# Kernel optimization log

Hardware: AMD Instinct MI355X
Metric: run time of the kernel (lower is better)

Reference implementation:

```python
import jax, jax.numpy as jnp
import numpy as np

DEFAULT_MASK_VALUE = -0.7 * float(jnp.finfo(jnp.dtype('float32')).max)


def setup_inputs() -> dict:
    key = jax.random.key(0)
    k1, k2, k3, k4 = jax.random.split(key, 4)
    B, T, NQ, NKV, D = 2, 2048, 32, 8, 128
    query = jax.random.normal(k1, (B, T, NQ, D), dtype=jnp.float32)
    k = jax.random.normal(k2, (B, T, NKV, D), dtype=jnp.float32)
    v = jax.random.normal(k3, (B, T, NKV, D), dtype=jnp.float32)
    # packed-sequence segment ids: sorted small ints so segments are contiguous
    decoder_segment_ids = jnp.sort(jax.random.randint(k4, (B, T), 0, 4), axis=-1).astype(jnp.int32)
    return {"query": query, "key": k, "value": v, "decoder_segment_ids": decoder_segment_ids}


def _generate_attention_mask(q_seq_len, kv_seq_len, decoder_segment_ids):
    # segment mask: [b, 1, 1, t, s]
    seg = (decoder_segment_ids[:, :, None] == decoder_segment_ids[:, None, :])[:, None, None, :, :]
    # causal mask: [1, 1, 1, t, s]
    row = jax.lax.broadcasted_iota(jnp.int32, (q_seq_len, kv_seq_len), 0)
    col = jax.lax.broadcasted_iota(jnp.int32, (q_seq_len, kv_seq_len), 1)
    causal = (col <= row)[None, None, None, :, :]
    mask = jnp.logical_and(seg, causal)
    return jnp.where(mask, 0.0, DEFAULT_MASK_VALUE)


def _apply_mask_to_logits(logits, mask):
    return jnp.where(mask >= DEFAULT_MASK_VALUE * 0.5, logits, DEFAULT_MASK_VALUE)


def reference(query, key, value, decoder_segment_ids):
    b, t, n, d = query.shape
    n_kv = key.shape[2]
    g = n // n_kv  # query heads per kv head (GQA)
    q = query.reshape(b, t, n_kv, g, d)
    # qk product (no internal sqrt(d) scaling, matching AttentionOp.qk_product)
    logits = jnp.einsum('btkgd,bskd->bkgts', q, key)  # [b, n_kv, g, t, s]
    mask = _generate_attention_mask(t, key.shape[1], decoder_segment_ids)
    logits = _apply_mask_to_logits(logits, mask)
    weights = jax.nn.softmax(logits, axis=-1).astype(query.dtype)
    out = jnp.einsum('bkgts,bskd->btkgd', weights, value)
    return out.reshape(b, t, n, d)
```

## Files before the change

### kernel.cpp

```cpp
#include <hip/hip_runtime.h>


typedef __bf16 bf16x8 __attribute__((ext_vector_type(8)));
typedef _Float16 f16x8 __attribute__((ext_vector_type(8)));
typedef float f32x4 __attribute__((ext_vector_type(4)));

#define B_   2
#define T_   2048
#define NQ_  32
#define NKV_ 8
#define D_   128

#define MASKV (-3.0e38f)
#define LOG2E 1.44269504f
#define TILE_US 8192
#define WS_TILES_BYTES ((size_t)B_ * NKV_ * (T_ / 32) * TILE_US * 2)
#define WS_NEED (WS_TILES_BYTES + (size_t)B_ * T_ * 4)

static __device__ __forceinline__ unsigned short f2bf(float x) {
    union { float f; unsigned int u; } c; c.f = x;
    unsigned int r = c.u + 0x7fffu + ((c.u >> 16) & 1u);
    return (unsigned short)(r >> 16);
}

union U8  { unsigned short us[8]; bf16x8 v; };
union H8  { _Float16 h[8]; f16x8 v; };

static __device__ __forceinline__ void dma16(const unsigned short* g, unsigned short* l) {
    __builtin_amdgcn_global_load_lds(
        (const __attribute__((address_space(1))) unsigned int*)g,
        (__attribute__((address_space(3))) unsigned int*)l, 16, 0, 0);
}

__global__ __launch_bounds__(256)
void prep(const float* __restrict__ kg, const float* __restrict__ vg,
          unsigned short* __restrict__ ws)
{
    const int tid = threadIdx.x;
    const int st  = blockIdx.x;
    const int kvh = blockIdx.y;
    const int b   = blockIdx.z;
    unsigned short* base = ws + ((size_t)((b * NKV_ + kvh) * (T_ / 32) + st)) * TILE_US;

    #pragma unroll
    for (int it = 0; it < 2; ++it) {
        int task = tid + it * 256;
        int r = task >> 4, c = task & 15;
        const float* kp = kg + (((size_t)(b * T_ + st * 32 + r)) * NKV_ + kvh) * D_ + c * 8;
        H8 hu;
        #pragma unroll
        for (int j = 0; j < 8; ++j) hu.h[j] = (_Float16)kp[j];
        int slot = r * 16 + (c ^ (r & 7));
        *(f16x8*)(base + slot * 8) = hu.v;
    }
    #pragma unroll
    for (int it = 0; it < 2; ++it) {
        int task = tid + it * 256;
        int d = task & 127, sc = task >> 7;
        const float* vp = vg + (((size_t)(b * T_ + st * 32 + sc * 8)) * NKV_ + kvh) * D_ + d;
        U8 pk;
        #pragma unroll
        for (int j = 0; j < 8; ++j) pk.us[j] = f2bf(vp[j * (NKV_ * D_)]);
        int slot = d * 4 + (sc ^ (d & 3));
        *(bf16x8*)(base + 4096 + slot * 8) = pk.v;
    }
}

__global__ __launch_bounds__(256)
void prep_sstart(const int* __restrict__ seg, int* __restrict__ sstart)
{
    int idx = blockIdx.x * 256 + threadIdx.x;
    int b = idx >> 11, t = idx & (T_ - 1);
    const int* sb = seg + b * T_;
    int target = sb[t];
    int lo = 0, hi = t;
    while (lo < hi) { int mid = (lo + hi) >> 1; if (sb[mid] < target) lo = mid + 1; else hi = mid; }
    sstart[idx] = lo;
}

__global__ __launch_bounds__(256)
void attn_fwd(const float* __restrict__ qg,
              const int* __restrict__ sstart,
              const unsigned short* __restrict__ ws,
              float* __restrict__ outg)
{
    __shared__ unsigned short sA[TILE_US];
    __shared__ unsigned short sB[TILE_US];
    __shared__ unsigned short sP[4][704];

    const int tid  = threadIdx.x;
    const int wave = tid >> 6;
    const int lane = tid & 63;
    const int qd   = lane >> 4;
    const int ln   = lane & 15;

    const int t0   = ((int)gridDim.x - 1 - (int)blockIdx.x) * 64;
    const int head = blockIdx.y;
    const int kvh  = head >> 2;
    const int b    = blockIdx.z;

    f16x8 qh[4], ql[4];
    {
        const float* qrow =
            qg + (((size_t)(b * T_ + (t0 + wave * 16 + ln)) * NQ_) + head) * D_;
        #pragma unroll
        for (int c = 0; c < 4; ++c) {
            float4 a  = *(const float4*)(qrow + c * 32 + qd * 8);
            float4 b2 = *(const float4*)(qrow + c * 32 + qd * 8 + 4);
            float xs[8] = {a.x, a.y, a.z, a.w, b2.x, b2.y, b2.z, b2.w};
            H8 hu, lu;
            #pragma unroll
            for (int j = 0; j < 8; ++j) {
                float x = xs[j] * LOG2E;
                _Float16 h = (_Float16)x;
                hu.h[j] = h;
                lu.h[j] = (_Float16)(x - (float)h);
            }
            qh[c] = hu.v; ql[c] = lu.v;
        }
    }

    int rowstart[4], trow[4];
    {
        int4 rs = *(const int4*)(sstart + b * T_ + t0 + wave * 16 + qd * 4);
        rowstart[0] = rs.x; rowstart[1] = rs.y; rowstart[2] = rs.z; rowstart[3] = rs.w;
        #pragma unroll
        for (int r = 0; r < 4; ++r) trow[r] = t0 + wave * 16 + qd * 4 + r;
    }
    int wave_rs_max = max(max(rowstart[0], rowstart[1]), max(rowstart[2], rowstart[3]));
    wave_rs_max = max(wave_rs_max, __shfl_xor(wave_rs_max, 16));
    wave_rs_max = max(wave_rs_max, __shfl_xor(wave_rs_max, 32));
    const int wave_row_min = t0 + wave * 16;

    const int tile0   = sstart[b * T_ + t0] >> 5;
    const int n_tiles = t0 / 32 + 2;

    f32x4 O[8];
    #pragma unroll
    for (int i = 0; i < 8; ++i) O[i] = (f32x4){0.f, 0.f, 0.f, 0.f};
    float l_lane[4] = {0.f, 0.f, 0.f, 0.f};

    const unsigned short* wsbase =
        ws + ((size_t)((b * NKV_ + kvh) * (T_ / 32))) * TILE_US;

    int koff[4];
    #pragma unroll
    for (int c = 0; c < 4; ++c)
        koff[c] = (ln * 16 + ((4 * c + qd) ^ (ln & 7))) * 8;
    const int vbase = (ln * 4 + (qd ^ (ln & 3))) * 8;
    const int pwbase = (qd * 4) * 40 + qd * 16 + ln;
    const int prbase = ln * 40 + (ln >> 2) * 16 + qd * 8;

#define STAGE(dst, tl) do {                                                    \
        const unsigned short* _tb = wsbase + (size_t)(tl) * TILE_US;           \
        _Pragma("unroll")                                                      \
        for (int _i = 0; _i < 4; ++_i)                                         \
            dma16(_tb + ((wave * 4 + _i) * 64 + lane) * 8,                     \
                  (dst) + (wave * 4 + _i) * 512);                              \
    } while (0)

#define COMPUTE(BUF, TL) do {                                                  \
        const unsigned short* _Kf = (BUF);                                     \
        const unsigned short* _Vt = (BUF) + 4096;                              \
        const int _s0 = (TL) * 32;                                             \
        f32x4 S0 = {0.f,0.f,0.f,0.f}, S1 = {0.f,0.f,0.f,0.f};                  \
        _Pragma("unroll")                                                      \
        for (int c = 0; c < 4; ++c) {                                          \
            f16x8 k0 = *(const f16x8*)(_Kf + koff[c]);                         \
            f16x8 k1 = *(const f16x8*)(_Kf + koff[c] + 2048);                  \
            S0 = __builtin_amdgcn_mfma_f32_16x16x32_f16(qh[c], k0, S0,0,0,0);  \
            S1 = __builtin_amdgcn_mfma_f32_16x16x32_f16(qh[c], k1, S1,0,0,0);  \
            S0 = __builtin_amdgcn_mfma_f32_16x16x32_f16(ql[c], k0, S0,0,0,0);  \
            S1 = __builtin_amdgcn_mfma_f32_16x16x32_f16(ql[c], k1, S1,0,0,0);  \
        }                                                                      \
        bf16x8 bv[8];                                                          \
        _Pragma("unroll")                                                      \
        for (int sub = 0; sub < 8; ++sub)                                      \
            bv[sub] = *(const bf16x8*)(_Vt + vbase + sub * 512);               \
        float p0[4], p1[4];                                                    \
        if (_s0 >= wave_rs_max && _s0 + 31 <= wave_row_min) {                  \
            _Pragma("unroll")                                                  \
            for (int r = 0; r < 4; ++r) {                                      \
                p0[r] = exp2f(S0[r]);                                          \
                p1[r] = exp2f(S1[r]);                                          \
            }                                                                  \
        } else {                                                               \
            _Pragma("unroll")                                                  \
            for (int r = 0; r < 4; ++r) {                                      \
                int sc0 = _s0 + ln, sc1 = _s0 + 16 + ln;                       \
                float sv0 = (sc0 >= rowstart[r] && sc0 <= trow[r]) ? S0[r] : MASKV; \
                float sv1 = (sc1 >= rowstart[r] && sc1 <= trow[r]) ? S1[r] : MASKV; \
                p0[r] = exp2f(sv0);                                            \
                p1[r] = exp2f(sv1);                                            \
            }                                                                  \
        }                                                                      \
        _Pragma("unroll")                                                      \
        for (int r = 0; r < 4; ++r) l_lane[r] += p0[r] + p1[r];                \
        {                                                                      \
            unsigned short* pw = sP[wave] + pwbase;                            \
            _Pragma("unroll")                                                  \
            for (int r = 0; r < 4; ++r) {                                      \
                pw[r * 40]      = f2bf(p0[r]);                                 \
                pw[r * 40 + 16] = f2bf(p1[r]);                                 \
            }                                                                  \
        }                                                                      \
        asm volatile("s_waitcnt lgkmcnt(0)" ::: "memory");                     \
        bf16x8 pa = *(const bf16x8*)(sP[wave] + prbase);                       \
        _Pragma("unroll")                                                      \
        for (int sub = 0; sub < 8; ++sub)                                      \
            O[sub] = __builtin_amdgcn_mfma_f32_16x16x32_bf16(pa, bv[sub], O[sub],0,0,0); \
    } while (0)

    int t = tile0;
    STAGE(sA, t);
    __syncthreads();
    while (t + 1 < n_tiles) {
        STAGE(sB, t + 1);
        COMPUTE(sA, t);
        __syncthreads();
        if (t + 2 < n_tiles) STAGE(sA, t + 2);
        COMPUTE(sB, t + 1);
        __syncthreads();
        t += 2;
    }
    if (t < n_tiles) COMPUTE(sA, t);

#undef STAGE
#undef COMPUTE

    float inv[4];
    #pragma unroll
    for (int r = 0; r < 4; ++r) {
        float l = l_lane[r];
        l += __shfl_xor(l, 1);
        l += __shfl_xor(l, 2);
        l += __shfl_xor(l, 4);
        l += __shfl_xor(l, 8);
        inv[r] = 1.0f / l;
    }
    #pragma unroll
    for (int sub = 0; sub < 8; ++sub) {
        #pragma unroll
        for (int r = 0; r < 4; ++r) {
            outg[(((size_t)(b * T_ + trow[r]) * NQ_) + head) * D_ + sub * 16 + ln] =
                O[sub][r] * inv[r];
        }
    }
}

#define KSTR 136
#define VSTR 40
#define PSTR 40
static __device__ __forceinline__ float bf2f(unsigned short h) {
    union { unsigned int u; float f; } c; c.u = (unsigned int)h << 16; return c.f;
}
__global__ __launch_bounds__(256)
void attn_fwd_fb(const float* __restrict__ qg,
                 const float* __restrict__ kg,
                 const float* __restrict__ vg,
                 const int* __restrict__ seg,
                 float* __restrict__ outg)
{
    __shared__ unsigned short sKh[32 * KSTR];
    __shared__ unsigned short sKl[32 * KSTR];
    __shared__ unsigned short sVt[128 * VSTR];
    __shared__ unsigned short sP[4][16 * PSTR];

    const int tid  = threadIdx.x;
    const int wave = tid >> 6;
    const int lane = tid & 63;
    const int qd   = lane >> 4;
    const int ln   = lane & 15;
    const int t0   = ((int)gridDim.x - 1 - (int)blockIdx.x) * 64;
    const int head = blockIdx.y;
    const int kvh  = head >> 2;
    const int b    = blockIdx.z;

    bf16x8 qh[4], ql[4];
    {
        const float* qrow =
            qg + (((size_t)(b * T_ + (t0 + wave * 16 + ln)) * NQ_) + head) * D_;
        #pragma unroll
        for (int c = 0; c < 4; ++c) {
            float4 a  = *(const float4*)(qrow + c * 32 + qd * 8);
            float4 b2 = *(const float4*)(qrow + c * 32 + qd * 8 + 4);
            float xs[8] = {a.x, a.y, a.z, a.w, b2.x, b2.y, b2.z, b2.w};
            U8 hu, lu;
            #pragma unroll
            for (int j = 0; j < 8; ++j) {
                unsigned short h = f2bf(xs[j]);
                hu.us[j] = h;
                lu.us[j] = f2bf(xs[j] - bf2f(h));
            }
            qh[c] = hu.v; ql[c] = lu.v;
        }
    }
    const int* sb = seg + (size_t)b * T_;
    int qseg[4];
    #pragma unroll
    for (int r = 0; r < 4; ++r) qseg[r] = sb[t0 + wave * 16 + qd * 4 + r];
    int tile0;
    {
        int target = sb[t0];
        int lo = 0, hi = t0;
        while (lo < hi) { int mid = (lo + hi) >> 1; if (sb[mid] < target) lo = mid + 1; else hi = mid; }
        tile0 = lo >> 5;
    }
    f32x4 O[8];
    #pragma unroll
    for (int i = 0; i < 8; ++i) O[i] = (f32x4){0.f, 0.f, 0.f, 0.f};
    float m_prev[4], l_lane[4];
    #pragma unroll
    for (int r = 0; r < 4; ++r) { m_prev[r] = MASKV; l_lane[r] = 0.f; }
    const int n_tiles = t0 / 32 + 2;

    for (int tile = tile0; tile < n_tiles; ++tile) {
        const int s0 = tile * 32;
        __syncthreads();
        #pragma unroll
        for (int it = 0; it < 2; ++it) {
            int task = tid + it * 256;
            int r = task >> 4, d = (task & 15) * 8;
            const float* kp = kg + (((size_t)(b * T_ + s0 + r) * NKV_) + kvh) * D_ + d;
            float4 a  = *(const float4*)(kp);
            float4 b2 = *(const float4*)(kp + 4);
            float xs[8] = {a.x, a.y, a.z, a.w, b2.x, b2.y, b2.z, b2.w};
            U8 hu, lu;
            #pragma unroll
            for (int j = 0; j < 8; ++j) {
                unsigned short h = f2bf(xs[j]);
                hu.us[j] = h;
                lu.us[j] = f2bf(xs[j] - bf2f(h));
            }
            *(bf16x8*)(sKh + r * KSTR + d) = hu.v;
            *(bf16x8*)(sKl + r * KSTR + d) = lu.v;
        }
        #pragma unroll
        for (int it = 0; it < 2; ++it) {
            int task = tid + it * 256;
            int d = task & 127, sg = task >> 7;
            const float* vp = vg + (((size_t)(b * T_ + s0 + sg * 8) * NKV_) + kvh) * D_ + d;
            U8 pk;
            #pragma unroll
            for (int j = 0; j < 8; ++j) pk.us[j] = f2bf(vp[j * (NKV_ * D_)]);
            *(bf16x8*)(sVt + d * VSTR + sg * 8) = pk.v;
        }
        __syncthreads();

        f32x4 S0 = {0.f,0.f,0.f,0.f}, S1 = {0.f,0.f,0.f,0.f};
        #pragma unroll
        for (int c = 0; c < 4; ++c) {
            bf16x8 kh0 = *(const bf16x8*)(sKh + ln * KSTR + c * 32 + qd * 8);
            bf16x8 kh1 = *(const bf16x8*)(sKh + (16 + ln) * KSTR + c * 32 + qd * 8);
            bf16x8 kl0 = *(const bf16x8*)(sKl + ln * KSTR + c * 32 + qd * 8);
            bf16x8 kl1 = *(const bf16x8*)(sKl + (16 + ln) * KSTR + c * 32 + qd * 8);
            S0 = __builtin_amdgcn_mfma_f32_16x16x32_bf16(qh[c], kh0, S0, 0, 0, 0);
            S1 = __builtin_amdgcn_mfma_f32_16x16x32_bf16(qh[c], kh1, S1, 0, 0, 0);
            S0 = __builtin_amdgcn_mfma_f32_16x16x32_bf16(qh[c], kl0, S0, 0, 0, 0);
            S1 = __builtin_amdgcn_mfma_f32_16x16x32_bf16(qh[c], kl1, S1, 0, 0, 0);
            S0 = __builtin_amdgcn_mfma_f32_16x16x32_bf16(ql[c], kh0, S0, 0, 0, 0);
            S1 = __builtin_amdgcn_mfma_f32_16x16x32_bf16(ql[c], kh1, S1, 0, 0, 0);
        }
        const int ks0 = sb[s0 + ln];
        const int ks1 = sb[s0 + 16 + ln];
        float p0[4], p1[4], alpha[4];
        #pragma unroll
        for (int r = 0; r < 4; ++r) {
            const int trow = t0 + wave * 16 + qd * 4 + r;
            float s0v = ((s0 + ln <= trow) && (ks0 == qseg[r])) ? S0[r] : MASKV;
            float s1v = ((s0 + 16 + ln <= trow) && (ks1 == qseg[r])) ? S1[r] : MASKV;
            float mx = fmaxf(s0v, s1v);
            mx = fmaxf(mx, __shfl_xor(mx, 1));
            mx = fmaxf(mx, __shfl_xor(mx, 2));
            mx = fmaxf(mx, __shfl_xor(mx, 4));
            mx = fmaxf(mx, __shfl_xor(mx, 8));
            const float mn = fmaxf(m_prev[r], mx);
            alpha[r] = __expf(m_prev[r] - mn);
            p0[r] = __expf(s0v - mn);
            p1[r] = __expf(s1v - mn);
            l_lane[r] = alpha[r] * l_lane[r] + p0[r] + p1[r];
            m_prev[r] = mn;
        }
        #pragma unroll
        for (int i = 0; i < 8; ++i) {
            O[i][0] *= alpha[0]; O[i][1] *= alpha[1];
            O[i][2] *= alpha[2]; O[i][3] *= alpha[3];
        }
        {
            unsigned short* pw = sP[wave] + (qd * 4) * PSTR + ln;
            #pragma unroll
            for (int r = 0; r < 4; ++r) {
                pw[r * PSTR]      = f2bf(p0[r]);
                pw[r * PSTR + 16] = f2bf(p1[r]);
            }
        }
        asm volatile("s_waitcnt lgkmcnt(0)" ::: "memory");
        bf16x8 pa = *(const bf16x8*)(sP[wave] + ln * PSTR + qd * 8);
        #pragma unroll
        for (int sub = 0; sub < 8; ++sub) {
            bf16x8 bv = *(const bf16x8*)(sVt + (sub * 16 + ln) * VSTR + qd * 8);
            O[sub] = __builtin_amdgcn_mfma_f32_16x16x32_bf16(pa, bv, O[sub], 0, 0, 0);
        }
    }
    float inv[4];
    #pragma unroll
    for (int r = 0; r < 4; ++r) {
        float l = l_lane[r];
        l += __shfl_xor(l, 1);
        l += __shfl_xor(l, 2);
        l += __shfl_xor(l, 4);
        l += __shfl_xor(l, 8);
        inv[r] = 1.0f / l;
    }
    #pragma unroll
    for (int sub = 0; sub < 8; ++sub) {
        #pragma unroll
        for (int r = 0; r < 4; ++r) {
            const int trow = t0 + wave * 16 + qd * 4 + r;
            outg[(((size_t)(b * T_ + trow) * NQ_) + head) * D_ + sub * 16 + ln] =
                O[sub][r] * inv[r];
        }
    }
}

extern "C" void kernel_launch(void* const* d_in, const int* in_sizes, int n_in,
                              void* d_out, int out_size, void* d_ws, size_t ws_size,
                              hipStream_t stream) {
    const float* q  = (const float*)d_in[0];
    const float* k  = (const float*)d_in[1];
    const float* v  = (const float*)d_in[2];
    const int*   sg = (const int*)d_in[3];
    float*       o  = (float*)d_out;
    if (ws_size >= WS_NEED) {
        unsigned short* ws = (unsigned short*)d_ws;
        int* sstart = (int*)((char*)d_ws + WS_TILES_BYTES);
        prep<<<dim3(T_ / 32, NKV_, B_), dim3(256), 0, stream>>>(k, v, ws);
        prep_sstart<<<dim3(B_ * T_ / 256), dim3(256), 0, stream>>>(sg, sstart);
        attn_fwd<<<dim3(T_ / 64, NQ_, B_), dim3(256), 0, stream>>>(q, sstart, ws, o);
    } else {
        attn_fwd_fb<<<dim3(T_ / 64, NQ_, B_), dim3(256), 0, stream>>>(q, k, v, sg, o);
    }
}
```

Baseline: 221.9 us.

## Compute transposed S^T via swapped MFMA operands and permlane swaps instead of LDS round-trip

Swaps the A/B operands of the QK MFMA so each lane holds one query row's scores across kv columns. The P fragment for the PV MFMA is then built in registers with bf16 packing and permlane32/16 swaps, which removes the per-tile LDS write, waitcnt and read of P. It also changes the V swizzle, uses per-lane row masking with a single l accumulator, adds s_setprio around the MFMA blocks, and sets an occupancy hint of 5 in launch bounds. The risk lies in the correctness of the permlane fragment mapping and possible register pressure under the tighter launch bound.

```diff
diff --git a/kernel.cpp b/kernel.cpp
--- a/kernel.cpp
+++ b/kernel.cpp
@@ -2,8 +2,10 @@
 
 
 typedef __bf16 bf16x8 __attribute__((ext_vector_type(8)));
+typedef __bf16 bf16x2 __attribute__((ext_vector_type(2)));
 typedef _Float16 f16x8 __attribute__((ext_vector_type(8)));
 typedef float f32x4 __attribute__((ext_vector_type(4)));
+typedef unsigned int uint2v __attribute__((ext_vector_type(2)));
 
 #define B_   2
 #define T_   2048
@@ -25,11 +27,30 @@
 
 union U8  { unsigned short us[8]; bf16x8 v; };
 union H8  { _Float16 h[8]; f16x8 v; };
+union PKW { bf16x2 h; unsigned int u; };
+union PA4 { unsigned int u[4]; bf16x8 v; };
 
 static __device__ __forceinline__ void dma16(const unsigned short* g, unsigned short* l) {
     __builtin_amdgcn_global_load_lds(
         (const __attribute__((address_space(1))) unsigned int*)g,
         (__attribute__((address_space(3))) unsigned int*)l, 16, 0, 0);
+}
+
+static __device__ __forceinline__ void pl32swap(unsigned int& a, unsigned int& b) {
+#if __has_builtin(__builtin_amdgcn_permlane32_swap)
+    uint2v t = __builtin_amdgcn_permlane32_swap(a, b, false, false);
+    a = t.x; b = t.y;
+#else
+    asm("s_nop 1\n\tv_permlane32_swap_b32 %0, %1" : "+v"(a), "+v"(b));
+#endif
+}
+static __device__ __forceinline__ void pl16swap(unsigned int& a, unsigned int& b) {
+#if __has_builtin(__builtin_amdgcn_permlane16_swap)
+    uint2v t = __builtin_amdgcn_permlane16_swap(a, b, false, false);
+    a = t.x; b = t.y;
+#else
+    asm("s_nop 1\n\tv_permlane16_swap_b32 %0, %1" : "+v"(a), "+v"(b));
+#endif
 }
 
 __global__ __launch_bounds__(256)
@@ -61,7 +82,7 @@
         U8 pk;
         #pragma unroll
         for (int j = 0; j < 8; ++j) pk.us[j] = f2bf(vp[j * (NKV_ * D_)]);
-        int slot = d * 4 + (sc ^ (d & 3));
+        int slot = d * 4 + (sc ^ ((d >> 1) & 3));
         *(bf16x8*)(base + 4096 + slot * 8) = pk.v;
     }
 }
@@ -78,7 +99,7 @@
     sstart[idx] = lo;
 }
 
-__global__ __launch_bounds__(256)
+__global__ __launch_bounds__(256, 5)
 void attn_fwd(const float* __restrict__ qg,
               const int* __restrict__ sstart,
               const unsigned short* __restrict__ ws,
@@ -86,7 +107,6 @@
 {
     __shared__ unsigned short sA[TILE_US];
     __shared__ unsigned short sB[TILE_US];
-    __shared__ unsigned short sP[4][704];
 
     const int tid  = threadIdx.x;
     const int wave = tid >> 6;
@@ -120,16 +140,13 @@
         }
     }
 
-    int rowstart[4], trow[4];
-    {
-        int4 rs = *(const int4*)(sstart + b * T_ + t0 + wave * 16 + qd * 4);
-        rowstart[0] = rs.x; rowstart[1] = rs.y; rowstart[2] = rs.z; rowstart[3] = rs.w;
-        #pragma unroll
-        for (int r = 0; r < 4; ++r) trow[r] = t0 + wave * 16 + qd * 4 + r;
-    }
-    int wave_rs_max = max(max(rowstart[0], rowstart[1]), max(rowstart[2], rowstart[3]));
-    wave_rs_max = max(wave_rs_max, __shfl_xor(wave_rs_max, 16));
-    wave_rs_max = max(wave_rs_max, __shfl_xor(wave_rs_max, 32));
+    const int trow_l = t0 + wave * 16 + ln;
+    const int rs_l   = sstart[b * T_ + trow_l];
+    int wave_rs_max = rs_l;
+    wave_rs_max = max(wave_rs_max, __shfl_xor(wave_rs_max, 1));
+    wave_rs_max = max(wave_rs_max, __shfl_xor(wave_rs_max, 2));
+    wave_rs_max = max(wave_rs_max, __shfl_xor(wave_rs_max, 4));
+    wave_rs_max = max(wave_rs_max, __shfl_xor(wave_rs_max, 8));
     const int wave_row_min = t0 + wave * 16;
 
     const int tile0   = sstart[b * T_ + t0] >> 5;
@@ -138,7 +155,7 @@
     f32x4 O[8];
     #pragma unroll
     for (int i = 0; i < 8; ++i) O[i] = (f32x4){0.f, 0.f, 0.f, 0.f};
-    float l_lane[4] = {0.f, 0.f, 0.f, 0.f};
+    float l_lane = 0.f;
 
     const unsigned short* wsbase =
         ws + ((size_t)((b * NKV_ + kvh) * (T_ / 32))) * TILE_US;
@@ -147,9 +164,7 @@
     #pragma unroll
     for (int c = 0; c < 4; ++c)
         koff[c] = (ln * 16 + ((4 * c + qd) ^ (ln & 7))) * 8;
-    const int vbase = (ln * 4 + (qd ^ (ln & 3))) * 8;
-    const int pwbase = (qd * 4) * 40 + qd * 16 + ln;
-    const int prbase = ln * 40 + (ln >> 2) * 16 + qd * 8;
+    const int vbase = (ln * 4 + (qd ^ ((ln >> 1) & 3))) * 8;
 
 #define STAGE(dst, tl) do {                                                    \
         const unsigned short* _tb = wsbase + (size_t)(tl) * TILE_US;           \
@@ -164,15 +179,17 @@
         const unsigned short* _Vt = (BUF) + 4096;                              \
         const int _s0 = (TL) * 32;                                             \
         f32x4 S0 = {0.f,0.f,0.f,0.f}, S1 = {0.f,0.f,0.f,0.f};                  \
+        __builtin_amdgcn_s_setprio(1);                                         \
         _Pragma("unroll")                                                      \
         for (int c = 0; c < 4; ++c) {                                          \
             f16x8 k0 = *(const f16x8*)(_Kf + koff[c]);                         \
             f16x8 k1 = *(const f16x8*)(_Kf + koff[c] + 2048);                  \
-            S0 = __builtin_amdgcn_mfma_f32_16x16x32_f16(qh[c], k0, S0,0,0,0);  \
-            S1 = __builtin_amdgcn_mfma_f32_16x16x32_f16(qh[c], k1, S1,0,0,0);  \
-            S0 = __builtin_amdgcn_mfma_f32_16x16x32_f16(ql[c], k0, S0,0,0,0);  \
-            S1 = __builtin_amdgcn_mfma_f32_16x16x32_f16(ql[c], k1, S1,0,0,0);  \
+            S0 = __builtin_amdgcn_mfma_f32_16x16x32_f16(k0, qh[c], S0,0,0,0);  \
+            S1 = __builtin_amdgcn_mfma_f32_16x16x32_f16(k1, qh[c], S1,0,0,0);  \
+            S0 = __builtin_amdgcn_mfma_f32_16x16x32_f16(k0, ql[c], S0,0,0,0);  \
+            S1 = __builtin_amdgcn_mfma_f32_16x16x32_f16(k1, ql[c], S1,0,0,0);  \
         }                                                                      \
+        __builtin_amdgcn_s_setprio(0);                                         \
         bf16x8 bv[8];                                                          \
         _Pragma("unroll")                                                      \
         for (int sub = 0; sub < 8; ++sub)                                      \
@@ -187,28 +204,31 @@
         } else {                                                               \
             _Pragma("unroll")                                                  \
             for (int r = 0; r < 4; ++r) {                                      \
-                int sc0 = _s0 + ln, sc1 = _s0 + 16 + ln;                       \
-                float sv0 = (sc0 >= rowstart[r] && sc0 <= trow[r]) ? S0[r] : MASKV; \
-                float sv1 = (sc1 >= rowstart[r] && sc1 <= trow[r]) ? S1[r] : MASKV; \
+                int kv0 = _s0 + qd * 4 + r;                                    \
+                int kv1 = kv0 + 16;                                            \
+                float sv0 = (kv0 >= rs_l && kv0 <= trow_l) ? S0[r] : MASKV;    \
+                float sv1 = (kv1 >= rs_l && kv1 <= trow_l) ? S1[r] : MASKV;    \
                 p0[r] = exp2f(sv0);                                            \
                 p1[r] = exp2f(sv1);                                            \
             }                                                                  \
         }                                                                      \
-        _Pragma("unroll")                                                      \
-        for (int r = 0; r < 4; ++r) l_lane[r] += p0[r] + p1[r];                \
-        {                                                                      \
-            unsigned short* pw = sP[wave] + pwbase;                            \
-            _Pragma("unroll")                                                  \
-            for (int r = 0; r < 4; ++r) {                                      \
-                pw[r * 40]      = f2bf(p0[r]);                                 \
-                pw[r * 40 + 16] = f2bf(p1[r]);                                 \
-            }                                                                  \
-        }                                                                      \
-        asm volatile("s_waitcnt lgkmcnt(0)" ::: "memory");                     \
-        bf16x8 pa = *(const bf16x8*)(sP[wave] + prbase);                       \
+        l_lane += (p0[0] + p0[1]) + (p0[2] + p0[3])                            \
+                + (p1[0] + p1[1]) + (p1[2] + p1[3]);                           \
+        PKW c0, c1, c2, c3;                                                    \
+        c0.h = (bf16x2){(__bf16)p0[0], (__bf16)p0[1]};                         \
+        c1.h = (bf16x2){(__bf16)p0[2], (__bf16)p0[3]};                         \
+        c2.h = (bf16x2){(__bf16)p1[0], (__bf16)p1[1]};                         \
+        c3.h = (bf16x2){(__bf16)p1[2], (__bf16)p1[3]};                         \
+        unsigned int w0 = c0.u, w1 = c1.u, w2 = c2.u, w3 = c3.u;               \
+        pl32swap(w0, w2); pl32swap(w1, w3);                                    \
+        pl16swap(w0, w2); pl16swap(w1, w3);                                    \
+        PA4 pw; pw.u[0] = w0; pw.u[1] = w1; pw.u[2] = w2; pw.u[3] = w3;        \
+        bf16x8 pa = pw.v;                                                      \
+        __builtin_amdgcn_s_setprio(1);                                         \
         _Pragma("unroll")                                                      \
         for (int sub = 0; sub < 8; ++sub)                                      \
             O[sub] = __builtin_amdgcn_mfma_f32_16x16x32_bf16(pa, bv[sub], O[sub],0,0,0); \
+        __builtin_amdgcn_s_setprio(0);                                         \
     } while (0)
 
     int t = tile0;
@@ -228,15 +248,16 @@
 #undef STAGE
 #undef COMPUTE
 
+    float l = l_lane;
+    l += __shfl_xor(l, 16);
+    l += __shfl_xor(l, 32);
+    const float invl = 1.0f / l;
+    int trow[4];
     float inv[4];
     #pragma unroll
     for (int r = 0; r < 4; ++r) {
-        float l = l_lane[r];
-        l += __shfl_xor(l, 1);
-        l += __shfl_xor(l, 2);
-        l += __shfl_xor(l, 4);
-        l += __shfl_xor(l, 8);
-        inv[r] = 1.0f / l;
+        trow[r] = t0 + wave * 16 + qd * 4 + r;
+        inv[r]  = __shfl(invl, qd * 4 + r);
     }
     #pragma unroll
     for (int sub = 0; sub < 8; ++sub) {
```

Result: slower. 440.0 us (+98.3%).
